# Performance work log

Hardware: AMD Instinct MI355X
Metric: run time of the kernel (lower is better)

Reference implementation:

```python
import jax, jax.numpy as jnp
import numpy as np

T, H, F = 4096, 4096, 14336

def setup_inputs() -> dict:
    key = jax.random.key(0)
    k1, k2, k3, k4 = jax.random.split(key, 4)
    s = 1.0 / np.sqrt(H)
    return {
        "x": jax.random.normal(k1, (T, H), dtype=jnp.float32),
        "expert_w1": jax.random.normal(k2, (H, F), dtype=jnp.float32) * s,
        "expert_v1": jax.random.normal(k3, (H, F), dtype=jnp.float32) * s,
        "expert_w2": jax.random.normal(k4, (H, F), dtype=jnp.float32) * s,
    }

def reference(x, expert_w1, expert_v1, expert_w2):
    # SwiGLU expert FFN: silu(x @ w1) * (x @ v1) @ w2.T
    gate_proj = jax.nn.silu(x @ expert_w1)          # [T, F]
    up_proj = x @ expert_v1                          # [T, F]
    down_proj = (gate_proj * up_proj) @ expert_w2.T  # [T, H]
    return down_proj
```

## Files before the change

### kernel.cpp

```cpp
#include <hip/hip_runtime.h>
#include <hip/hip_bf16.h>
#include <stdint.h>

#define TT 4096
#define HH 4096
#define FF 14336
#define NCAT (2 * FF)

typedef __attribute__((ext_vector_type(8))) short bf16x8;
typedef __attribute__((ext_vector_type(4))) float f32x4;

__device__ __forceinline__ unsigned short f32_to_bf16(float f) {
    union { float f; unsigned int u; } v; v.f = f;
    unsigned int r = v.u + 0x7FFFu + ((v.u >> 16) & 1u);
    return (unsigned short)(r >> 16);
}

#define GLOAD16(g, l)                                                          \
    __builtin_amdgcn_global_load_lds(                                          \
        (const __attribute__((address_space(1))) void*)(g),                    \
        (__attribute__((address_space(3))) void*)(l), 16, 0, 0)

__global__ void cvt_lin(const float* __restrict__ in,
                        unsigned short* __restrict__ out, long n4) {
    long stride = (long)gridDim.x * blockDim.x;
    for (long i = (long)blockIdx.x * blockDim.x + threadIdx.x; i < n4; i += stride) {
        float4 v = *(const float4*)(in + i * 4);
        ushort4 o;
        o.x = f32_to_bf16(v.x); o.y = f32_to_bf16(v.y);
        o.z = f32_to_bf16(v.z); o.w = f32_to_bf16(v.w);
        *(ushort4*)(out + i * 4) = o;
    }
}

__global__ void cvt_tri(const float* __restrict__ in,
                        unsigned short* __restrict__ out, int off) {
    __shared__ float tile[64][65];
    int bh = blockIdx.x & 63;
    int bf = blockIdx.x >> 6;
    int t = threadIdx.x;
    int r16 = t >> 4;
    int c4 = (t & 15) * 4;
#pragma unroll
    for (int it = 0; it < 4; ++it) {
        int h = r16 + it * 16;
        float4 v = *(const float4*)(in + (size_t)(bh * 64 + h) * FF + bf * 64 + c4);
        tile[h][c4 + 0] = v.x; tile[h][c4 + 1] = v.y;
        tile[h][c4 + 2] = v.z; tile[h][c4 + 3] = v.w;
    }
    __syncthreads();
#pragma unroll
    for (int it = 0; it < 4; ++it) {
        int f = r16 + it * 16;
        int fg = bf * 64 + f;
        int row_out = ((fg >> 4) << 5) + (fg & 15) + off;
        ushort4 o;
        o.x = f32_to_bf16(tile[c4 + 0][f]);
        o.y = f32_to_bf16(tile[c4 + 1][f]);
        o.z = f32_to_bf16(tile[c4 + 2][f]);
        o.w = f32_to_bf16(tile[c4 + 3][f]);
        *(ushort4*)(out + (size_t)row_out * HH + bh * 64 + c4) = o;
    }
}


#define STG_A(BUF, SLOT, TILE) do {                                            \
    char* d_ = lsA + (((BUF)*2 + (SLOT)) << 14) + tid * 16;                    \
    GLOAD16(sA[SLOT][0] + (size_t)(TILE) * 64, d_);                            \
    GLOAD16(sA[SLOT][1] + (size_t)(TILE) * 64, d_ + 8192);                     \
  } while (0)

#define STG_B(BUF, SLOT, TILE) do {                                            \
    char* d_ = lsB + (((BUF)*2 + (SLOT)) << 14) + tid * 16;                    \
    GLOAD16(sB[SLOT][0] + (size_t)(TILE) * 64, d_);                            \
    GLOAD16(sB[SLOT][1] + (size_t)(TILE) * 64, d_ + 8192);                     \
  } while (0)

#define PHASE(BUF, MQ, NQ, STAGES, FENCE) do {                                 \
    const char* pA_ = lsA + (((BUF)*2 + (MQ)) << 14);                          \
    const char* pB_ = lsB + (((BUF)*2 + (NQ)) << 14);                          \
    bf16x8 af_[4][2], bf_[2][2];                                               \
    _Pragma("unroll") for (int i_ = 0; i_ < 4; ++i_)                           \
    _Pragma("unroll") for (int k_ = 0; k_ < 2; ++k_)                           \
      af_[i_][k_] = *(const bf16x8*)(pA_ + ((((wr*64 + i_*16 + fr) << 7) + k_*64 + kg2) ^ lmask)); \
    _Pragma("unroll") for (int j_ = 0; j_ < 2; ++j_)                           \
    _Pragma("unroll") for (int k_ = 0; k_ < 2; ++k_)                           \
      bf_[j_][k_] = *(const bf16x8*)(pB_ + ((((wc*32 + j_*16 + fr) << 7) + k_*64 + kg2) ^ lmask)); \
    STAGES;                                                                    \
    asm volatile("" ::: "memory");                                             \
    __builtin_amdgcn_s_barrier();                                              \
    asm volatile("" ::: "memory");                                             \
    __builtin_amdgcn_s_setprio(1);                                             \
    _Pragma("unroll") for (int i_ = 0; i_ < 4; ++i_)                           \
    _Pragma("unroll") for (int j_ = 0; j_ < 2; ++j_)                           \
    _Pragma("unroll") for (int k_ = 0; k_ < 2; ++k_)                           \
      acc[MQ][i_][NQ][j_] = __builtin_amdgcn_mfma_f32_16x16x32_bf16(           \
          af_[i_][k_], bf_[j_][k_], acc[MQ][i_][NQ][j_], 0, 0, 0);             \
    __builtin_amdgcn_s_setprio(0);                                             \
    FENCE;                                                                     \
    asm volatile("" ::: "memory");                                             \
    __builtin_amdgcn_s_barrier();                                              \
    asm volatile("" ::: "memory");                                             \
  } while (0)

#define VMC4 asm volatile("s_waitcnt vmcnt(4)" ::: "memory")
#define VMC0 asm volatile("s_waitcnt vmcnt(0)" ::: "memory")

#define GEMM8_CORE(A_, LDA_, B_, LDB_, NT_)                                    \
  extern __shared__ char smem[];                                               \
  char* const lsA = smem;                                                      \
  char* const lsB = smem + 65536;                                              \
  const int tid = threadIdx.x;                                                 \
  const int lane = tid & 63;                                                   \
  const int wid = tid >> 6;                                                    \
  const int wr = wid >> 2;                                                     \
  const int wc = wid & 3;                                                      \
  const int fr = lane & 15;                                                    \
  const int kg2 = ((lane >> 4) & 3) << 4;                                      \
  const int lmask = (fr & 6) << 4;                                             \
  f32x4 acc[2][4][2][2];                                                       \
  _Pragma("unroll") for (int a_ = 0; a_ < 2; ++a_)                             \
  _Pragma("unroll") for (int b_ = 0; b_ < 4; ++b_)                             \
  _Pragma("unroll") for (int c_ = 0; c_ < 2; ++c_)                             \
  _Pragma("unroll") for (int d_ = 0; d_ < 2; ++d_)                             \
    acc[a_][b_][c_][d_] = (f32x4){0.f, 0.f, 0.f, 0.f};                         \
  const unsigned short* sA[2][2];                                              \
  const unsigned short* sB[2][2];                                              \
  _Pragma("unroll") for (int c_ = 0; c_ < 2; ++c_) {                           \
    int d_ = (tid + 512 * c_) * 16;                                            \
    int p_ = d_ ^ (((d_ >> 8) & 3) << 5);                                      \
    int prow = p_ >> 7, pcol = (p_ & 127) >> 1;                                \
    _Pragma("unroll") for (int s_ = 0; s_ < 2; ++s_) {                         \
      int grA = m0 + ((prow >> 6) & 1) * 128 + s_ * 64 + (prow & 63);          \
      sA[s_][c_] = (A_) + (size_t)grA * (LDA_) + pcol;                         \
      int grB = n0 + (prow >> 5) * 64 + s_ * 32 + (prow & 31);                 \
      sB[s_][c_] = (B_) + (size_t)grB * (LDB_) + pcol;                         \
    }                                                                          \
  }                                                                            \
  \
  STG_A(0, 0, 0); STG_B(0, 0, 0); STG_B(0, 1, 0); STG_A(0, 1, 0);              \
  STG_A(1, 0, 1); STG_B(1, 0, 1);                                              \
  VMC4;                                                                        \
  __builtin_amdgcn_s_barrier();                                                \
  asm volatile("" ::: "memory");                                               \
  const int niter = (NT_) / 2;                                                 \
  for (int I = 0; I < niter - 1; ++I) {                                        \
    const int t = 2 * I;                                                       \
    PHASE(0, 0, 0, STG_B(1, 1, t + 1), );                                      \
    PHASE(0, 0, 1, STG_A(1, 1, t + 1), );                                      \
    PHASE(0, 1, 0, STG_A(0, 0, t + 2), );                                      \
    PHASE(0, 1, 1, STG_B(0, 0, t + 2), VMC4);                                  \
    PHASE(1, 0, 0, STG_B(0, 1, t + 2), );                                      \
    PHASE(1, 0, 1, STG_A(0, 1, t + 2), );                                      \
    PHASE(1, 1, 0, STG_A(1, 0, t + 3), );                                      \
    PHASE(1, 1, 1, STG_B(1, 0, t + 3), VMC4);                                  \
  }                                                                            \
  {                                                                            \
    const int t = (NT_) - 2;                                                   \
    PHASE(0, 0, 0, STG_B(1, 1, t + 1), );                                      \
    PHASE(0, 0, 1, STG_A(1, 1, t + 1), );                                      \
    PHASE(0, 1, 0, , );                                                        \
    PHASE(0, 1, 1, , VMC0);                                                    \
    PHASE(1, 0, 0, , );                                                        \
    PHASE(1, 0, 1, , );                                                        \
    PHASE(1, 1, 0, , );                                                        \
    PHASE(1, 1, 1, , );                                                        \
  }

__global__ __launch_bounds__(512, 2) void gemm_swiglu(
    const unsigned short* __restrict__ Xb,
    const unsigned short* __restrict__ Wcat,
    unsigned short* __restrict__ Act) {
    const int NWG = (TT / 256) * (NCAT / 256);
    int lid = (blockIdx.x & 7) * (NWG / 8) + (blockIdx.x >> 3);
    const int m0 = (lid & 15) * 256;
    const int n0 = (lid >> 4) * 256;

    GEMM8_CORE(Xb, HH, Wcat, HH, HH / 64)

    const int dm = ((lane >> 4) & 3) * 4;
    const int dn = lane & 15;
#pragma unroll
    for (int mq = 0; mq < 2; ++mq)
#pragma unroll
        for (int i = 0; i < 4; ++i)
#pragma unroll
            for (int nq = 0; nq < 2; ++nq) {
                int rowb = m0 + wr * 128 + mq * 64 + i * 16 + dm;
                int col = (n0 + wc * 64 + nq * 32) / 2 + dn;
                f32x4 g4 = acc[mq][i][nq][0];
                f32x4 u4 = acc[mq][i][nq][1];
#pragma unroll
                for (int r = 0; r < 4; ++r) {
                    float g = g4[r], u = u4[r];
                    float s = g * u / (1.0f + __expf(-g));
                    Act[(size_t)(rowb + r) * FF + col] = f32_to_bf16(s);
                }
            }
}

__global__ __launch_bounds__(512, 2) void gemm_down(
    const unsigned short* __restrict__ Act,
    const unsigned short* __restrict__ W2b,
    float* __restrict__ Out) {
    const int NWG = (TT / 256) * (HH / 256);
    int lid = (blockIdx.x & 7) * (NWG / 8) + (blockIdx.x >> 3);
    const int m0 = (lid & 15) * 256;
    const int n0 = (lid >> 4) * 256;

    GEMM8_CORE(Act, FF, W2b, FF, FF / 64)

    const int dm = ((lane >> 4) & 3) * 4;
    const int dn = lane & 15;
#pragma unroll
    for (int mq = 0; mq < 2; ++mq)
#pragma unroll
        for (int i = 0; i < 4; ++i)
#pragma unroll
            for (int nq = 0; nq < 2; ++nq)
#pragma unroll
                for (int j = 0; j < 2; ++j) {
                    int rowb = m0 + wr * 128 + mq * 64 + i * 16 + dm;
                    int col = n0 + wc * 64 + nq * 32 + j * 16 + dn;
                    f32x4 v = acc[mq][i][nq][j];
#pragma unroll
                    for (int r = 0; r < 4; ++r)
                        Out[(size_t)(rowb + r) * HH + col] = v[r];
                }
}

extern "C" void kernel_launch(void* const* d_in, const int* in_sizes, int n_in,
                              void* d_out, int out_size, void* d_ws, size_t ws_size,
                              hipStream_t stream) {
    const float* x  = (const float*)d_in[0];
    const float* w1 = (const float*)d_in[1];
    const float* v1 = (const float*)d_in[2];
    const float* w2 = (const float*)d_in[3];
    float* out = (float*)d_out;

    unsigned short* xb   = (unsigned short*)d_ws;
    unsigned short* wcat = xb + (size_t)TT * HH;
    unsigned short* w2b  = wcat + (size_t)NCAT * HH;
    unsigned short* act  = w2b + (size_t)HH * FF;

    hipFuncSetAttribute((const void*)gemm_swiglu,
                        hipFuncAttributeMaxDynamicSharedMemorySize, 131072);
    hipFuncSetAttribute((const void*)gemm_down,
                        hipFuncAttributeMaxDynamicSharedMemorySize, 131072);

    cvt_lin<<<2048, 256, 0, stream>>>(x, xb, (long)TT * HH / 4);
    cvt_lin<<<2048, 256, 0, stream>>>(w2, w2b, (long)HH * FF / 4);
    cvt_tri<<<(HH / 64) * (FF / 64), 256, 0, stream>>>(w1, wcat, 0);
    cvt_tri<<<(HH / 64) * (FF / 64), 256, 0, stream>>>(v1, wcat, 16);

    gemm_swiglu<<<(TT / 256) * (NCAT / 256), 512, 131072, stream>>>(xb, wcat, act);
    gemm_down<<<(TT / 256) * (HH / 256), 512, 131072, stream>>>(act, w2b, out);
}
```

Before: 1.473 ms.

## Reuse LDS fragments across quadrants and restructure GEMM prefetch schedule

The 8-wave GEMM main loop now keeps A and B fragment registers live across the four quadrant phases, in the order (0,0),(1,0),(1,1),(0,1). Each phase reads only one new A or B fragment set from LDS instead of both. The global-to-LDS staging is rescheduled so that a whole K-tile buffer is refilled after its quadrants are consumed: the prologue prefetches two full tiles and the loop waits with vmcnt(8). This lowers LDS read traffic per MFMA and simplifies the pipeline, at the cost of more live VGPRs under the 512x2 launch bounds, which risks spills or lower occupancy.

After: 2.356 ms. +59.9%, slower.

```diff
diff --git a/kernel.cpp b/kernel.cpp
--- a/kernel.cpp
+++ b/kernel.cpp
@@ -76,35 +76,58 @@
     GLOAD16(sB[SLOT][1] + (size_t)(TILE) * 64, d_ + 8192);                     \
   } while (0)
 
-#define PHASE(BUF, MQ, NQ, STAGES, FENCE) do {                                 \
+#define READ_A(DST, BUF, MQ) do {                                              \
     const char* pA_ = lsA + (((BUF)*2 + (MQ)) << 14);                          \
-    const char* pB_ = lsB + (((BUF)*2 + (NQ)) << 14);                          \
-    bf16x8 af_[4][2], bf_[2][2];                                               \
     _Pragma("unroll") for (int i_ = 0; i_ < 4; ++i_)                           \
     _Pragma("unroll") for (int k_ = 0; k_ < 2; ++k_)                           \
-      af_[i_][k_] = *(const bf16x8*)(pA_ + ((((wr*64 + i_*16 + fr) << 7) + k_*64 + kg2) ^ lmask)); \
+      DST[i_][k_] = *(const bf16x8*)(pA_ + ((((wr*64 + i_*16 + fr) << 7) + k_*64 + kg2) ^ lmask)); \
+  } while (0)
+
+#define READ_B(DST, BUF, NQ) do {                                              \
+    const char* pB_ = lsB + (((BUF)*2 + (NQ)) << 14);                          \
     _Pragma("unroll") for (int j_ = 0; j_ < 2; ++j_)                           \
     _Pragma("unroll") for (int k_ = 0; k_ < 2; ++k_)                           \
-      bf_[j_][k_] = *(const bf16x8*)(pB_ + ((((wc*32 + j_*16 + fr) << 7) + k_*64 + kg2) ^ lmask)); \
-    STAGES;                                                                    \
-    asm volatile("" ::: "memory");                                             \
-    __builtin_amdgcn_s_barrier();                                              \
-    asm volatile("" ::: "memory");                                             \
-    __builtin_amdgcn_s_setprio(1);                                             \
+      DST[j_][k_] = *(const bf16x8*)(pB_ + ((((wc*32 + j_*16 + fr) << 7) + k_*64 + kg2) ^ lmask)); \
+  } while (0)
+
+#define MFMA_Q(MQ, NQ, AF, BF)                                                 \
     _Pragma("unroll") for (int i_ = 0; i_ < 4; ++i_)                           \
     _Pragma("unroll") for (int j_ = 0; j_ < 2; ++j_)                           \
     _Pragma("unroll") for (int k_ = 0; k_ < 2; ++k_)                           \
       acc[MQ][i_][NQ][j_] = __builtin_amdgcn_mfma_f32_16x16x32_bf16(           \
-          af_[i_][k_], bf_[j_][k_], acc[MQ][i_][NQ][j_], 0, 0, 0);             \
-    __builtin_amdgcn_s_setprio(0);                                             \
-    FENCE;                                                                     \
+          AF[i_][k_], BF[j_][k_], acc[MQ][i_][NQ][j_], 0, 0, 0)
+
+#define BAR do {                                                               \
     asm volatile("" ::: "memory");                                             \
     __builtin_amdgcn_s_barrier();                                              \
     asm volatile("" ::: "memory");                                             \
   } while (0)
 
-#define VMC4 asm volatile("s_waitcnt vmcnt(4)" ::: "memory")
+#define VMC8 asm volatile("s_waitcnt vmcnt(8)" ::: "memory")
 #define VMC0 asm volatile("s_waitcnt vmcnt(0)" ::: "memory")
+
+#define PH(READS, STAGES, MQ, NQ, AF, BF, FENCE) do {                          \
+    READS;                                                                     \
+    STAGES;                                                                    \
+    BAR;                                                                       \
+    __builtin_amdgcn_s_setprio(1);                                             \
+    MFMA_Q(MQ, NQ, AF, BF);                                                    \
+    __builtin_amdgcn_s_setprio(0);                                             \
+    FENCE;                                                                     \
+    BAR;                                                                       \
+  } while (0)
+
+#define HALF_STG(BUF, TS, F4)                                                  \
+    PH(READ_A(af0, BUF, 0); READ_B(bf0, BUF, 0), , 0, 0, af0, bf0, );          \
+    PH(READ_A(af1, BUF, 1), STG_A(BUF, 0, TS), 1, 0, af1, bf0, );              \
+    PH(READ_B(bf1, BUF, 1), STG_B(BUF, 0, TS), 1, 1, af1, bf1, );              \
+    PH(, STG_A(BUF, 1, TS); STG_B(BUF, 1, TS), 0, 1, af0, bf1, F4);
+
+#define HALF_NOSTG(BUF, F4)                                                    \
+    PH(READ_A(af0, BUF, 0); READ_B(bf0, BUF, 0), , 0, 0, af0, bf0, );          \
+    PH(READ_A(af1, BUF, 1), , 1, 0, af1, bf0, );                               \
+    PH(READ_B(bf1, BUF, 1), , 1, 1, af1, bf1, );                               \
+    PH(, , 0, 1, af0, bf1, F4);
 
 #define GEMM8_CORE(A_, LDA_, B_, LDB_, NT_)                                    \
   extern __shared__ char smem[];                                               \
@@ -124,6 +147,7 @@
   _Pragma("unroll") for (int c_ = 0; c_ < 2; ++c_)                             \
   _Pragma("unroll") for (int d_ = 0; d_ < 2; ++d_)                             \
     acc[a_][b_][c_][d_] = (f32x4){0.f, 0.f, 0.f, 0.f};                         \
+  bf16x8 af0[4][2], af1[4][2], bf0[2][2], bf1[2][2];                           \
   const unsigned short* sA[2][2];                                              \
   const unsigned short* sB[2][2];                                              \
   _Pragma("unroll") for (int c_ = 0; c_ < 2; ++c_) {                           \
@@ -137,35 +161,20 @@
       sB[s_][c_] = (B_) + (size_t)grB * (LDB_) + pcol;                         \
     }                                                                          \
   }                                                                            \
-  \
-  STG_A(0, 0, 0); STG_B(0, 0, 0); STG_B(0, 1, 0); STG_A(0, 1, 0);              \
-  STG_A(1, 0, 1); STG_B(1, 0, 1);                                              \
-  VMC4;                                                                        \
+        \
+  STG_A(0, 0, 0); STG_B(0, 0, 0); STG_A(0, 1, 0); STG_B(0, 1, 0);              \
+  STG_A(1, 0, 1); STG_B(1, 0, 1); STG_A(1, 1, 1); STG_B(1, 1, 1);              \
+  VMC8;                                                                        \
   __builtin_amdgcn_s_barrier();                                                \
   asm volatile("" ::: "memory");                                               \
   const int niter = (NT_) / 2;                                                 \
   for (int I = 0; I < niter - 1; ++I) {                                        \
     const int t = 2 * I;                                                       \
-    PHASE(0, 0, 0, STG_B(1, 1, t + 1), );                                      \
-    PHASE(0, 0, 1, STG_A(1, 1, t + 1), );                                      \
-    PHASE(0, 1, 0, STG_A(0, 0, t + 2), );                                      \
-    PHASE(0, 1, 1, STG_B(0, 0, t + 2), VMC4);                                  \
-    PHASE(1, 0, 0, STG_B(0, 1, t + 2), );                                      \
-    PHASE(1, 0, 1, STG_A(0, 1, t + 2), );                                      \
-    PHASE(1, 1, 0, STG_A(1, 0, t + 3), );                                      \
-    PHASE(1, 1, 1, STG_B(1, 0, t + 3), VMC4);                                  \
+    HALF_STG(0, t + 2, VMC8)                                                   \
+    HALF_STG(1, t + 3, VMC8)                                                   \
   }                                                                            \
-  {                                                                            \
-    const int t = (NT_) - 2;                                                   \
-    PHASE(0, 0, 0, STG_B(1, 1, t + 1), );                                      \
-    PHASE(0, 0, 1, STG_A(1, 1, t + 1), );                                      \
-    PHASE(0, 1, 0, , );                                                        \
-    PHASE(0, 1, 1, , VMC0);                                                    \
-    PHASE(1, 0, 0, , );                                                        \
-    PHASE(1, 0, 1, , );                                                        \
-    PHASE(1, 1, 0, , );                                                        \
-    PHASE(1, 1, 1, , );                                                        \
-  }
+  HALF_NOSTG(0, VMC0)                                                          \
+  HALF_NOSTG(1, )
 
 __global__ __launch_bounds__(512, 2) void gemm_swiglu(
     const unsigned short* __restrict__ Xb,
```
